# Kernel optimization log

Hardware: AMD Instinct MI355X
Metric: run time of the kernel (lower is better)

The kernel has to match this reference:

```python
import jax, jax.numpy as jnp
import numpy as np

# instant-ngp HashGrid config
L, F, LOG2_T, BASE, SCALE = 16, 2, 19, 16, 1.3819
T = 1 << LOG2_T
B = 1048576
_CORNERS = np.array([[(c >> 0) & 1, (c >> 1) & 1, (c >> 2) & 1] for c in range(8)], np.int32)  # [8,3]


def hash_encode(x, grid):
    # x: [B,3] in [0,1]; grid: [L,T,F] hash tables. Trilinear interp of hashed corner features.
    corners = jnp.asarray(_CORNERS)
    outs = []
    for l in range(L):  # fixed small level loop
        res = float(np.floor(BASE * SCALE ** l))
        pos = x * res
        pos0 = jnp.floor(pos)
        w = pos - pos0                                            # [B,3] trilinear fracs
        idx = pos0.astype(jnp.uint32)[:, None, :] + corners.astype(jnp.uint32)[None]  # [B,8,3]
        h = (idx[..., 0] * jnp.uint32(1)) ^ (idx[..., 1] * jnp.uint32(2654435761)) ^ (idx[..., 2] * jnp.uint32(805459861))
        h = (h & jnp.uint32(T - 1)).astype(jnp.int32)             # [B,8]
        wc = jnp.prod(jnp.where(corners[None] == 1, w[:, None, :], 1.0 - w[:, None, :]), axis=-1)  # [B,8]
        outs.append(jnp.einsum('bcf,bc->bf', grid[l][h], wc))     # [B,F]
    return jnp.concatenate(outs, axis=-1)                         # [B, L*F]


def sh16(d):
    # Spherical harmonics degree 4 (tcnn coefficients), input in [-1,1]^3
    x, y, z = d[:, 0], d[:, 1], d[:, 2]
    x2, y2, z2 = x * x, y * y, z * z
    xy, yz, xz = x * y, y * z, x * z
    one = jnp.ones_like(x)
    return jnp.stack([
        0.28209479177387814 * one,
        -0.48860251190291987 * y,
        0.48860251190291987 * z,
        -0.48860251190291987 * x,
        1.0925484305920792 * xy,
        -1.0925484305920792 * yz,
        0.94617469575755997 * z2 - 0.31539156525251999,
        -1.0925484305920792 * xz,
        0.54627421529603959 * (x2 - y2),
        0.59004358992664352 * y * (-3.0 * x2 + y2),
        2.8906114426405538 * xy * z,
        0.45704579946446572 * y * (1.0 - 5.0 * z2),
        0.3731763325901154 * z * (5.0 * z2 - 3.0),
        0.45704579946446572 * x * (1.0 - 5.0 * z2),
        1.4453057213202769 * z * (x2 - y2),
        0.59004358992664352 * x * (-x2 + 3.0 * y2),
    ], axis=-1)


def setup_inputs() -> dict:
    key = jax.random.key(0)
    ks = jax.random.split(key, 20)
    gdim, shid, chid = 15, 64, 64
    in_color = gdim + 16 + 16  # geo_feat + SH + latent = 47

    def lin(k, o, i):
        k1, k2 = jax.random.split(k)
        bound = 1.0 / np.sqrt(i)
        return (jax.random.uniform(k1, (o, i), jnp.float32, -bound, bound),
                jax.random.uniform(k2, (o,), jnp.float32, -bound, bound))

    sw0, sb0 = lin(ks[0], shid, L * F)
    sw1, sb1 = lin(ks[1], shid, shid)
    sw2, sb2 = lin(ks[2], 1 + gdim, shid)
    cw0, cb0 = lin(ks[3], chid, in_color)
    cw1, cb1 = lin(ks[4], chid, chid)
    cw2, cb2 = lin(ks[5], chid, chid)
    cw3, cb3 = lin(ks[6], 3, chid)
    return {
        'x': jax.random.uniform(ks[7], (B, 3), jnp.float32),
        'd': jax.random.normal(ks[8], (B, 3), jnp.float32),
        'n': jax.random.randint(ks[9], (B,), 0, 100, jnp.int32),
        'grid': jax.random.uniform(ks[10], (L, T, F), jnp.float32, -1e-4, 1e-4),
        'latent_emb': jax.random.normal(ks[11], (100, 16), jnp.float32) * 0.01,
        'sw0': sw0, 'sb0': sb0, 'sw1': sw1, 'sb1': sb1, 'sw2': sw2, 'sb2': sb2,
        'cw0': cw0, 'cb0': cb0, 'cw1': cw1, 'cb1': cb1, 'cw2': cw2, 'cb2': cb2, 'cw3': cw3, 'cb3': cb3,
    }


def reference(x, d, n, grid, latent_emb, sw0, sb0, sw1, sb1, sw2, sb2,
              cw0, cb0, cw1, cb1, cw2, cb2, cw3, cb3):
    h = hash_encode(x, grid)                         # [B, 32]
    h = jax.nn.relu(h @ sw0.T + sb0)
    h = jax.nn.relu(h @ sw1.T + sb1)
    s = h @ sw2.T + sb2                              # [B, 1+geo]
    sigma, geo = s[:, 0], s[:, 1:]
    dd = ((d + 1.0) * 0.5) * 2.0 - 1.0               # module maps d->[0,1]; tcnn SH maps back to [-1,1]
    cin = jnp.concatenate([geo, sh16(dd), latent_emb[n]], axis=-1)  # [B, 47]
    c = jax.nn.relu(cin @ cw0.T + cb0)
    c = jax.nn.relu(c @ cw1.T + cb1)
    c = jax.nn.relu(c @ cw2.T + cb2)
    color = jax.nn.sigmoid(c @ cw3.T + cb3)          # [B, 3]
    return sigma, color
```

## Files before the change

kernel.cpp:

```cpp
#include <hip/hip_runtime.h>
#include <hip/hip_bf16.h>
#include <hip/hip_fp8.h>


#define TBL   524288
#define TMASK (TBL - 1)
#define MPB   512
#define NTHR  1024

#define FP8_SCALE     1048576.0f
#define FP8_INV_SCALE 9.5367431640625e-7f

typedef __bf16 bf16x8 __attribute__((ext_vector_type(8)));
typedef float  f32x4  __attribute__((ext_vector_type(4)));

__device__ const float RES_TAB[16] = {
    16.f, 22.f, 30.f, 42.f, 58.f, 80.f, 111.f, 153.f,
    212.f, 294.f, 406.f, 561.f, 775.f, 1072.f, 1481.f, 2047.f
};

__device__ __forceinline__ unsigned short f2bf(float f) {
    __hip_bfloat16 h = __float2bfloat16(f);
    unsigned short u;
    __builtin_memcpy(&u, &h, 2);
    return u;
}
__device__ __forceinline__ unsigned pack2(float a, float b) {
    return (unsigned)f2bf(a) | ((unsigned)f2bf(b) << 16);
}

__device__ __forceinline__ float fp8_dec(unsigned b) {
#if defined(__has_builtin) && __has_builtin(__builtin_amdgcn_cvt_f32_fp8)
    return __builtin_amdgcn_cvt_f32_fp8((int)b, 0);
#else
    const unsigned e = (b >> 3) & 0xF, m = b & 7;
    float v = e ? ldexpf((float)(8 + m), (int)e - 10) : ldexpf((float)m, -9);
    return (b & 0x80) ? -v : v;
#endif
}
__device__ __forceinline__ unsigned short fp8_pair(float a, float b) {
#if defined(__has_builtin) && __has_builtin(__builtin_amdgcn_cvt_pk_fp8_f32)
    return (unsigned short)(__builtin_amdgcn_cvt_pk_fp8_f32(a, b, 0, false) & 0xffff);
#else
    __hip_fp8_e4m3 qa(a), qb(b);
    return (unsigned short)((unsigned)qa.__x | ((unsigned)qb.__x << 8));
#endif
}

__global__ void __launch_bounds__(1024) grid_to_fp8(
    const float2* __restrict__ g, unsigned short* __restrict__ o, int n)
{
    const int i = blockIdx.x * 1024 + threadIdx.x;
    if (i < n) {
        const float2 v = g[i];
        o[i] = fp8_pair(v.x * FP8_SCALE, v.y * FP8_SCALE);
    }
}

template<int KS, int NT, bool RELU>
__device__ __forceinline__ void mlp_layer(
    const unsigned short* a0, int s0,
    const unsigned short* a1, int s1,
    const unsigned short* __restrict__ W, int ws,
    const float* __restrict__ bias,
    unsigned short* outp, int os,
    int wave, int lane)
{
    const int lr = lane & 15, lg = lane >> 4;
    bf16x8 bfr[NT][KS];
#pragma unroll
    for (int nt = 0; nt < NT; ++nt)
#pragma unroll
        for (int ks = 0; ks < KS; ++ks)
            bfr[nt][ks] = *reinterpret_cast<const bf16x8*>(W + (nt * 16 + lr) * ws + ks * 32 + lg * 8);

#pragma unroll
    for (int mt = 0; mt < 2; ++mt) {
        const int R = wave * 32 + mt * 16;
        bf16x8 afr[KS];
        afr[0] = *reinterpret_cast<const bf16x8*>(a0 + (R + lr) * s0 + lg * 8);
        if constexpr (KS > 1)
            afr[1] = *reinterpret_cast<const bf16x8*>(a1 + (R + lr) * s1 + lg * 8);

        f32x4 acc[NT] = {};
#pragma unroll
        for (int nt = 0; nt < NT; ++nt)
#pragma unroll
            for (int ks = 0; ks < KS; ++ks)
                acc[nt] = __builtin_amdgcn_mfma_f32_16x16x32_bf16(afr[ks], bfr[nt][ks], acc[nt], 0, 0, 0);

#pragma unroll
        for (int nt = 0; nt < NT; ++nt) {
            const float b = bias[nt * 16 + lr];
#pragma unroll
            for (int r = 0; r < 4; ++r) {
                float v = acc[nt][r] + b;
                if (RELU) v = fmaxf(v, 0.f);
                outp[(R + lg * 4 + r) * os + nt * 16 + lr] = f2bf(v);
            }
        }
    }
}

template<int GM>
__global__ void __launch_bounds__(NTHR, 4) nerf_fused(
    const float* __restrict__ x, const float* __restrict__ dvec,
    const int*   __restrict__ nidx, const void* __restrict__ grid,
    const float* __restrict__ latent,
    const float* __restrict__ sw0, const float* __restrict__ sb0,
    const float* __restrict__ sw1, const float* __restrict__ sb1,
    const float* __restrict__ sw2, const float* __restrict__ sb2,
    const float* __restrict__ cw0, const float* __restrict__ cb0,
    const float* __restrict__ cw1, const float* __restrict__ cb1,
    const float* __restrict__ cw2, const float* __restrict__ cb2,
    const float* __restrict__ cw3, const float* __restrict__ cb3,
    float* __restrict__ out, int B)
{
    __shared__ __align__(16) unsigned short sW0[64 * 40];
    __shared__ __align__(16) unsigned short sW1[64 * 72];
    __shared__ __align__(16) unsigned short sW2[16 * 72];
    __shared__ __align__(16) unsigned short sC0[64 * 72];
    __shared__ __align__(16) unsigned short sC1[64 * 72];
    __shared__ __align__(16) unsigned short sC2[64 * 72];
    __shared__ __align__(16) unsigned short sC3[16 * 72];
    __shared__ float sB[352];
    __shared__ __align__(16) unsigned short sAct[MPB * 72];

    const int tid = threadIdx.x;

    for (int i = tid; i < 64 * 40; i += NTHR) { int n = i / 40, k = i % 40; sW0[i] = f2bf(k < 32 ? sw0[n * 32 + k] : 0.f); }
    for (int i = tid; i < 64 * 72; i += NTHR) { int n = i / 72, k = i % 72; sW1[i] = f2bf(k < 64 ? sw1[n * 64 + k] : 0.f); }
    for (int i = tid; i < 16 * 72; i += NTHR) { int n = i / 72, k = i % 72; sW2[i] = f2bf(k < 64 ? sw2[n * 64 + k] : 0.f); }
    for (int i = tid; i < 64 * 72; i += NTHR) {
        int n = i / 72, k = i % 72;
        float v = 0.f;
        if (k < 15) v = cw0[n * 47 + k];
        else if (k >= 32 && k < 64) v = cw0[n * 47 + k - 17];
        sC0[i] = f2bf(v);
    }
    for (int i = tid; i < 64 * 72; i += NTHR) { int n = i / 72, k = i % 72; sC1[i] = f2bf(k < 64 ? cw1[n * 64 + k] : 0.f); }
    for (int i = tid; i < 64 * 72; i += NTHR) { int n = i / 72, k = i % 72; sC2[i] = f2bf(k < 64 ? cw2[n * 64 + k] : 0.f); }
    for (int i = tid; i < 16 * 72; i += NTHR) { int n = i / 72, k = i % 72; sC3[i] = f2bf((n < 3 && k < 64) ? cw3[n * 64 + k] : 0.f); }
    if (tid < 64) {
        sB[tid]       = sb0[tid];
        sB[64 + tid]  = sb1[tid];
        sB[144 + tid] = cb0[tid];
        sB[208 + tid] = cb1[tid];
        sB[272 + tid] = cb2[tid];
    }
    if (tid < 16) {
        sB[128 + tid] = sb2[tid];
        sB[336 + tid] = (tid < 3) ? cb3[tid] : 0.f;
    }

    const int p  = tid & (MPB - 1);
    const int hv = tid >> 9;
    const long long P = (long long)blockIdx.x * MPB + p;

    if constexpr (GM == 1) {
        const float x0 = x[3 * P + 0], x1 = x[3 * P + 1], x2 = x[3 * P + 2];
        const unsigned short* __restrict__ tf = reinterpret_cast<const unsigned short*>(grid);
#pragma unroll 2
        for (int lp = 0; lp < 4; ++lp) {
            unsigned idx[2][8];
            float wxa[2][2], wya[2][2], wza[2][2];
#pragma unroll
            for (int s = 0; s < 2; ++s) {
                const int l = hv * 8 + lp * 2 + s;
                const float res = RES_TAB[l];
                const float px = x0 * res, py = x1 * res, pz = x2 * res;
                const float fx = floorf(px), fy = floorf(py), fz = floorf(pz);
                const float wx = px - fx, wy = py - fy, wz = pz - fz;
                const unsigned ix = (unsigned)fx, iy = (unsigned)fy, iz = (unsigned)fz;
                const unsigned hx0 = ix, hx1 = ix + 1u;
                const unsigned hy0 = iy * 2654435761u, hy1 = (iy + 1u) * 2654435761u;
                const unsigned hz0 = iz * 805459861u,  hz1 = (iz + 1u) * 805459861u;
                const unsigned base = (unsigned)l * (unsigned)TBL;
#pragma unroll
                for (int c = 0; c < 8; ++c) {
                    const unsigned h = ((c & 1) ? hx1 : hx0) ^ (((c >> 1) & 1) ? hy1 : hy0)
                                     ^ (((c >> 2) & 1) ? hz1 : hz0);
                    idx[s][c] = base + (h & TMASK);
                }
                wxa[s][0] = 1.f - wx; wxa[s][1] = wx;
                wya[s][0] = 1.f - wy; wya[s][1] = wy;
                wza[s][0] = 1.f - wz; wza[s][1] = wz;
            }
            unsigned short u[2][8];
#pragma unroll
            for (int s = 0; s < 2; ++s)
#pragma unroll
                for (int c = 0; c < 8; ++c)
                    u[s][c] = tf[idx[s][c]];
#pragma unroll
            for (int s = 0; s < 2; ++s) {
                float f0 = 0.f, f1 = 0.f;
#pragma unroll
                for (int c = 0; c < 8; ++c) {
                    const float wc = wxa[s][c & 1] * wya[s][(c >> 1) & 1] * wza[s][(c >> 2) & 1];
                    const unsigned uu = u[s][c];
                    f0 = fmaf(fp8_dec(uu & 0xffu), wc, f0);
                    f1 = fmaf(fp8_dec((uu >> 8) & 0xffu), wc, f1);
                }
                const int l = hv * 8 + lp * 2 + s;
                *reinterpret_cast<unsigned*>(&sAct[p * 72 + 2 * l]) =
                    pack2(f0 * FP8_INV_SCALE, f1 * FP8_INV_SCALE);
            }
        }
    } else {
        const float x0 = x[3 * P + 0], x1 = x[3 * P + 1], x2 = x[3 * P + 2];
        const float2* __restrict__ gtab = reinterpret_cast<const float2*>(grid);
#pragma unroll 2
        for (int ll = 0; ll < 8; ++ll) {
            const int l = hv * 8 + ll;
            const float res = RES_TAB[l];
            const float px = x0 * res, py = x1 * res, pz = x2 * res;
            const float fx = floorf(px), fy = floorf(py), fz = floorf(pz);
            const float wx = px - fx, wy = py - fy, wz = pz - fz;
            const unsigned ix = (unsigned)fx, iy = (unsigned)fy, iz = (unsigned)fz;
            const unsigned hx[2] = { ix, ix + 1u };
            const unsigned hy[2] = { iy * 2654435761u, (iy + 1u) * 2654435761u };
            const unsigned hz[2] = { iz * 805459861u, (iz + 1u) * 805459861u };
            const float2* tl = gtab + (size_t)l * TBL;
            float2 g[8];
#pragma unroll
            for (int c = 0; c < 8; ++c) {
                const unsigned h = hx[c & 1] ^ hy[(c >> 1) & 1] ^ hz[(c >> 2) & 1];
                g[c] = tl[h & TMASK];
            }
            const float wxa[2] = { 1.f - wx, wx }, wya[2] = { 1.f - wy, wy }, wza[2] = { 1.f - wz, wz };
            float f0 = 0.f, f1 = 0.f;
#pragma unroll
            for (int c = 0; c < 8; ++c) {
                const float wc = wxa[c & 1] * wya[(c >> 1) & 1] * wza[(c >> 2) & 1];
                f0 = fmaf(g[c].x, wc, f0);
                f1 = fmaf(g[c].y, wc, f1);
            }
            *reinterpret_cast<unsigned*>(&sAct[p * 72 + 2 * l]) = pack2(f0, f1);
        }
    }

    unsigned creg0, creg1, creg2, creg3, creg4, creg5, creg6, creg7;
    if (hv == 0) {
        const float X = dvec[3 * P + 0], Y = dvec[3 * P + 1], Z = dvec[3 * P + 2];
        const float x2 = X * X, y2 = Y * Y, z2 = Z * Z, xy = X * Y, yz = Y * Z, xz = X * Z;
        const float s0 = 0.28209479177387814f;
        const float s1 = -0.48860251190291987f * Y;
        const float s2 = 0.48860251190291987f * Z;
        const float s3 = -0.48860251190291987f * X;
        const float s4 = 1.0925484305920792f * xy;
        const float s5 = -1.0925484305920792f * yz;
        const float s6 = 0.94617469575756f * z2 - 0.31539156525252f;
        const float s7 = -1.0925484305920792f * xz;
        const float s8 = 0.5462742152960396f * (x2 - y2);
        const float s9 = 0.5900435899266435f * Y * (-3.f * x2 + y2);
        const float s10 = 2.890611442640554f * xy * Z;
        const float s11 = 0.4570457994644657f * Y * (1.f - 5.f * z2);
        const float s12 = 0.3731763325901154f * Z * (5.f * z2 - 3.f);
        const float s13 = 0.4570457994644657f * X * (1.f - 5.f * z2);
        const float s14 = 1.445305721320277f * Z * (x2 - y2);
        const float s15 = 0.5900435899266435f * X * (-x2 + 3.f * y2);
        creg0 = pack2(s0, s1);   creg1 = pack2(s2, s3);
        creg2 = pack2(s4, s5);   creg3 = pack2(s6, s7);
        creg4 = pack2(s8, s9);   creg5 = pack2(s10, s11);
        creg6 = pack2(s12, s13); creg7 = pack2(s14, s15);
    } else {
        const int id = nidx[P];
        const float4* lp = reinterpret_cast<const float4*>(latent + 16 * id);
        const float4 a = lp[0], b = lp[1], c = lp[2], d4 = lp[3];
        creg0 = pack2(a.x, a.y); creg1 = pack2(a.z, a.w);
        creg2 = pack2(b.x, b.y); creg3 = pack2(b.z, b.w);
        creg4 = pack2(c.x, c.y); creg5 = pack2(c.z, c.w);
        creg6 = pack2(d4.x, d4.y); creg7 = pack2(d4.z, d4.w);
    }

    __syncthreads();

    const int lane = tid & 63;
    const int wave = tid >> 6;

    mlp_layer<1, 4, true>(sAct, 72, nullptr, 0,    sW0, 40, sB + 0,  sAct, 72, wave, lane);
    mlp_layer<2, 4, true>(sAct, 72, sAct + 32, 72, sW1, 72, sB + 64, sAct, 72, wave, lane);

    {
        const int lr = lane & 15, lg = lane >> 4;
        const bf16x8 b0 = *reinterpret_cast<const bf16x8*>(sW2 + lr * 72 + lg * 8);
        const bf16x8 b1 = *reinterpret_cast<const bf16x8*>(sW2 + lr * 72 + 32 + lg * 8);
        const float bb = sB[128 + lr];
#pragma unroll
        for (int mt = 0; mt < 2; ++mt) {
            const int R = wave * 32 + mt * 16;
            const bf16x8 a0 = *reinterpret_cast<const bf16x8*>(sAct + (R + lr) * 72 + lg * 8);
            const bf16x8 a1 = *reinterpret_cast<const bf16x8*>(sAct + (R + lr) * 72 + 32 + lg * 8);
            f32x4 acc = {};
            acc = __builtin_amdgcn_mfma_f32_16x16x32_bf16(a0, b0, acc, 0, 0, 0);
            acc = __builtin_amdgcn_mfma_f32_16x16x32_bf16(a1, b1, acc, 0, 0, 0);
#pragma unroll
            for (int r = 0; r < 4; ++r) {
                const float v = acc[r] + bb;
                const int row = R + lg * 4 + r;
                if (lr == 0) {
                    out[(long long)blockIdx.x * MPB + row] = v;
                    sAct[row * 72 + 31] = 0;
                } else {
                    sAct[row * 72 + lr - 1] = f2bf(v);
                }
                sAct[row * 72 + 15 + lr] = 0;
            }
        }
    }

    __syncthreads();

    {
        unsigned* c2 = reinterpret_cast<unsigned*>(&sAct[p * 72 + 32 + hv * 16]);
        c2[0] = creg0; c2[1] = creg1; c2[2] = creg2; c2[3] = creg3;
        c2[4] = creg4; c2[5] = creg5; c2[6] = creg6; c2[7] = creg7;
    }

    __syncthreads();

    mlp_layer<2, 4, true>(sAct, 72, sAct + 32, 72, sC0, 72, sB + 144, sAct, 72, wave, lane);
    mlp_layer<2, 4, true>(sAct, 72, sAct + 32, 72, sC1, 72, sB + 208, sAct, 72, wave, lane);
    mlp_layer<2, 4, true>(sAct, 72, sAct + 32, 72, sC2, 72, sB + 272, sAct, 72, wave, lane);

    {
        const int lr = lane & 15, lg = lane >> 4;
        const bf16x8 b0 = *reinterpret_cast<const bf16x8*>(sC3 + lr * 72 + lg * 8);
        const bf16x8 b1 = *reinterpret_cast<const bf16x8*>(sC3 + lr * 72 + 32 + lg * 8);
        const float bb = sB[336 + lr];
#pragma unroll
        for (int mt = 0; mt < 2; ++mt) {
            const int R = wave * 32 + mt * 16;
            const bf16x8 a0 = *reinterpret_cast<const bf16x8*>(sAct + (R + lr) * 72 + lg * 8);
            const bf16x8 a1 = *reinterpret_cast<const bf16x8*>(sAct + (R + lr) * 72 + 32 + lg * 8);
            f32x4 acc = {};
            acc = __builtin_amdgcn_mfma_f32_16x16x32_bf16(a0, b0, acc, 0, 0, 0);
            acc = __builtin_amdgcn_mfma_f32_16x16x32_bf16(a1, b1, acc, 0, 0, 0);
            if (lr < 3) {
#pragma unroll
                for (int r = 0; r < 4; ++r) {
                    const float v = acc[r] + bb;
                    const long long row = (long long)blockIdx.x * MPB + R + lg * 4 + r;
                    out[(long long)B + row * 3 + lr] = 1.f / (1.f + __expf(-v));
                }
            }
        }
    }
}

extern "C" void kernel_launch(void* const* d_in, const int* in_sizes, int n_in,
                              void* d_out, int out_size, void* d_ws, size_t ws_size,
                              hipStream_t stream) {
    const float* x    = (const float*)d_in[0];
    const float* dv   = (const float*)d_in[1];
    const int*   n    = (const int*)d_in[2];
    const float* grid = (const float*)d_in[3];
    const float* lat  = (const float*)d_in[4];
    const float* sw0  = (const float*)d_in[5];
    const float* sb0  = (const float*)d_in[6];
    const float* sw1  = (const float*)d_in[7];
    const float* sb1  = (const float*)d_in[8];
    const float* sw2  = (const float*)d_in[9];
    const float* sb2  = (const float*)d_in[10];
    const float* cw0  = (const float*)d_in[11];
    const float* cb0  = (const float*)d_in[12];
    const float* cw1  = (const float*)d_in[13];
    const float* cb1  = (const float*)d_in[14];
    const float* cw2  = (const float*)d_in[15];
    const float* cb2  = (const float*)d_in[16];
    const float* cw3  = (const float*)d_in[17];
    const float* cb3  = (const float*)d_in[18];

    const int B = in_sizes[2];
    const int nblocks = B / MPB;

    const int nent = 16 * TBL;
    const size_t ws_need = (size_t)nent * 2;

    if (ws_size >= ws_need) {
        grid_to_fp8<<<dim3((nent + 1023) / 1024), dim3(1024), 0, stream>>>(
            reinterpret_cast<const float2*>(grid), (unsigned short*)d_ws, nent);
        nerf_fused<1><<<dim3(nblocks), dim3(NTHR), 0, stream>>>(
            x, dv, n, (const void*)d_ws, lat,
            sw0, sb0, sw1, sb1, sw2, sb2,
            cw0, cb0, cw1, cb1, cw2, cb2, cw3, cb3,
            (float*)d_out, B);
    } else {
        nerf_fused<0><<<dim3(nblocks), dim3(NTHR), 0, stream>>>(
            x, dv, n, (const void*)grid, lat,
            sw0, sb0, sw1, sb1, sw2, sb2,
            cw0, cb0, cw1, cb1, cw2, cb2, cw3, cb3,
            (float*)d_out, B);
    }
}
```

Before: 621.6 us.

## Pre-pack MLP weights once globally and halve block size for occupancy

Adds a single-block kernel that converts and pads all MLP weights and biases to bf16/float in workspace once, so the main kernel no longer stages ~48KB of weights into shared memory per block. The fused kernel now reads weight fragments directly from global/L2 and uses only the activation buffer in LDS. It also halves points per block to 256 with 512 threads and raises launch bounds to 8 blocks per CU. The aim is to cut per-block setup cost and LDS pressure so more blocks stay resident to hide the hash-gather latency. In exchange, weight operands are fetched from cache on every MFMA layer instead of LDS.

```diff
diff --git a/kernel.cpp b/kernel.cpp
--- a/kernel.cpp
+++ b/kernel.cpp
@@ -5,8 +5,20 @@
 
 #define TBL   524288
 #define TMASK (TBL - 1)
-#define MPB   512
-#define NTHR  1024
+#define MPB   256
+#define NTHR  512
+
+#define GRID_SHORTS (16 * TBL)
+#define GRID_BYTES  (GRID_SHORTS * 2)
+#define OW0 0
+#define OW1 2560
+#define OC0 7168
+#define OC1 11776
+#define OC2 16384
+#define OW2 20992
+#define OC3 22144
+#define OBF 23296
+#define WS_NEED ((size_t)GRID_BYTES + 48000)
 
 #define FP8_SCALE     1048576.0f
 #define FP8_INV_SCALE 9.5367431640625e-7f
@@ -54,6 +66,44 @@
     if (i < n) {
         const float2 v = g[i];
         o[i] = fp8_pair(v.x * FP8_SCALE, v.y * FP8_SCALE);
+    }
+}
+
+__global__ void __launch_bounds__(1024) pack_weights(
+    unsigned short* __restrict__ w,
+    const float* __restrict__ sw0, const float* __restrict__ sb0,
+    const float* __restrict__ sw1, const float* __restrict__ sb1,
+    const float* __restrict__ sw2, const float* __restrict__ sb2,
+    const float* __restrict__ cw0, const float* __restrict__ cb0,
+    const float* __restrict__ cw1, const float* __restrict__ cb1,
+    const float* __restrict__ cw2, const float* __restrict__ cb2,
+    const float* __restrict__ cw3, const float* __restrict__ cb3)
+{
+    const int tid = threadIdx.x;
+    for (int i = tid; i < 64 * 40; i += 1024) { int n = i / 40, k = i % 40; w[OW0 + i] = f2bf(k < 32 ? sw0[n * 32 + k] : 0.f); }
+    for (int i = tid; i < 64 * 72; i += 1024) { int n = i / 72, k = i % 72; w[OW1 + i] = f2bf(k < 64 ? sw1[n * 64 + k] : 0.f); }
+    for (int i = tid; i < 64 * 72; i += 1024) {
+        int n = i / 72, k = i % 72;
+        float v = 0.f;
+        if (k < 15) v = cw0[n * 47 + k];
+        else if (k >= 32 && k < 64) v = cw0[n * 47 + k - 17];
+        w[OC0 + i] = f2bf(v);
+    }
+    for (int i = tid; i < 64 * 72; i += 1024) { int n = i / 72, k = i % 72; w[OC1 + i] = f2bf(k < 64 ? cw1[n * 64 + k] : 0.f); }
+    for (int i = tid; i < 64 * 72; i += 1024) { int n = i / 72, k = i % 72; w[OC2 + i] = f2bf(k < 64 ? cw2[n * 64 + k] : 0.f); }
+    for (int i = tid; i < 16 * 72; i += 1024) { int n = i / 72, k = i % 72; w[OW2 + i] = f2bf(k < 64 ? sw2[n * 64 + k] : 0.f); }
+    for (int i = tid; i < 16 * 72; i += 1024) { int n = i / 72, k = i % 72; w[OC3 + i] = f2bf((n < 3 && k < 64) ? cw3[n * 64 + k] : 0.f); }
+    float* gB = reinterpret_cast<float*>(w + OBF);
+    if (tid < 64) {
+        gB[tid]       = sb0[tid];
+        gB[64 + tid]  = sb1[tid];
+        gB[144 + tid] = cb0[tid];
+        gB[208 + tid] = cb1[tid];
+        gB[272 + tid] = cb2[tid];
+    }
+    if (tid < 16) {
+        gB[128 + tid] = sb2[tid];
+        gB[336 + tid] = (tid < 3) ? cb3[tid] : 0.f;
     }
 }
 
@@ -102,64 +152,25 @@
     }
 }
 
-template<int GM>
-__global__ void __launch_bounds__(NTHR, 4) nerf_fused(
+__global__ void __launch_bounds__(NTHR, 8) nerf_fused_v8(
     const float* __restrict__ x, const float* __restrict__ dvec,
-    const int*   __restrict__ nidx, const void* __restrict__ grid,
+    const int*   __restrict__ nidx,
+    const unsigned short* __restrict__ gfp8,
+    const unsigned short* __restrict__ wz,
     const float* __restrict__ latent,
-    const float* __restrict__ sw0, const float* __restrict__ sb0,
-    const float* __restrict__ sw1, const float* __restrict__ sb1,
-    const float* __restrict__ sw2, const float* __restrict__ sb2,
-    const float* __restrict__ cw0, const float* __restrict__ cb0,
-    const float* __restrict__ cw1, const float* __restrict__ cb1,
-    const float* __restrict__ cw2, const float* __restrict__ cb2,
-    const float* __restrict__ cw3, const float* __restrict__ cb3,
     float* __restrict__ out, int B)
 {
-    __shared__ __align__(16) unsigned short sW0[64 * 40];
-    __shared__ __align__(16) unsigned short sW1[64 * 72];
-    __shared__ __align__(16) unsigned short sW2[16 * 72];
-    __shared__ __align__(16) unsigned short sC0[64 * 72];
-    __shared__ __align__(16) unsigned short sC1[64 * 72];
-    __shared__ __align__(16) unsigned short sC2[64 * 72];
-    __shared__ __align__(16) unsigned short sC3[16 * 72];
-    __shared__ float sB[352];
     __shared__ __align__(16) unsigned short sAct[MPB * 72];
 
     const int tid = threadIdx.x;
-
-    for (int i = tid; i < 64 * 40; i += NTHR) { int n = i / 40, k = i % 40; sW0[i] = f2bf(k < 32 ? sw0[n * 32 + k] : 0.f); }
-    for (int i = tid; i < 64 * 72; i += NTHR) { int n = i / 72, k = i % 72; sW1[i] = f2bf(k < 64 ? sw1[n * 64 + k] : 0.f); }
-    for (int i = tid; i < 16 * 72; i += NTHR) { int n = i / 72, k = i % 72; sW2[i] = f2bf(k < 64 ? sw2[n * 64 + k] : 0.f); }
-    for (int i = tid; i < 64 * 72; i += NTHR) {
-        int n = i / 72, k = i % 72;
-        float v = 0.f;
-        if (k < 15) v = cw0[n * 47 + k];
-        else if (k >= 32 && k < 64) v = cw0[n * 47 + k - 17];
-        sC0[i] = f2bf(v);
-    }
-    for (int i = tid; i < 64 * 72; i += NTHR) { int n = i / 72, k = i % 72; sC1[i] = f2bf(k < 64 ? cw1[n * 64 + k] : 0.f); }
-    for (int i = tid; i < 64 * 72; i += NTHR) { int n = i / 72, k = i % 72; sC2[i] = f2bf(k < 64 ? cw2[n * 64 + k] : 0.f); }
-    for (int i = tid; i < 16 * 72; i += NTHR) { int n = i / 72, k = i % 72; sC3[i] = f2bf((n < 3 && k < 64) ? cw3[n * 64 + k] : 0.f); }
-    if (tid < 64) {
-        sB[tid]       = sb0[tid];
-        sB[64 + tid]  = sb1[tid];
-        sB[144 + tid] = cb0[tid];
-        sB[208 + tid] = cb1[tid];
-        sB[272 + tid] = cb2[tid];
-    }
-    if (tid < 16) {
-        sB[128 + tid] = sb2[tid];
-        sB[336 + tid] = (tid < 3) ? cb3[tid] : 0.f;
-    }
+    const float* __restrict__ gB = reinterpret_cast<const float*>(wz + OBF);
 
     const int p  = tid & (MPB - 1);
-    const int hv = tid >> 9;
+    const int hv = tid >> 8;
     const long long P = (long long)blockIdx.x * MPB + p;
 
-    if constexpr (GM == 1) {
+    {
         const float x0 = x[3 * P + 0], x1 = x[3 * P + 1], x2 = x[3 * P + 2];
-        const unsigned short* __restrict__ tf = reinterpret_cast<const unsigned short*>(grid);
 #pragma unroll 2
         for (int lp = 0; lp < 4; ++lp) {
             unsigned idx[2][8];
@@ -170,7 +181,7 @@
                 const float res = RES_TAB[l];
                 const float px = x0 * res, py = x1 * res, pz = x2 * res;
                 const float fx = floorf(px), fy = floorf(py), fz = floorf(pz);
-                const float wx = px - fx, wy = py - fy, wz = pz - fz;
+                const float wx = px - fx, wy = py - fy, wz2 = pz - fz;
                 const unsigned ix = (unsigned)fx, iy = (unsigned)fy, iz = (unsigned)fz;
                 const unsigned hx0 = ix, hx1 = ix + 1u;
                 const unsigned hy0 = iy * 2654435761u, hy1 = (iy + 1u) * 2654435761u;
@@ -184,14 +195,14 @@
                 }
                 wxa[s][0] = 1.f - wx; wxa[s][1] = wx;
                 wya[s][0] = 1.f - wy; wya[s][1] = wy;
-                wza[s][0] = 1.f - wz; wza[s][1] = wz;
+                wza[s][0] = 1.f - wz2; wza[s][1] = wz2;
             }
             unsigned short u[2][8];
 #pragma unroll
             for (int s = 0; s < 2; ++s)
 #pragma unroll
                 for (int c = 0; c < 8; ++c)
-                    u[s][c] = tf[idx[s][c]];
+                    u[s][c] = gfp8[idx[s][c]];
 #pragma unroll
             for (int s = 0; s < 2; ++s) {
                 float f0 = 0.f, f1 = 0.f;
@@ -206,37 +217,6 @@
                 *reinterpret_cast<unsigned*>(&sAct[p * 72 + 2 * l]) =
                     pack2(f0 * FP8_INV_SCALE, f1 * FP8_INV_SCALE);
             }
-        }
-    } else {
-        const float x0 = x[3 * P + 0], x1 = x[3 * P + 1], x2 = x[3 * P + 2];
-        const float2* __restrict__ gtab = reinterpret_cast<const float2*>(grid);
-#pragma unroll 2
-        for (int ll = 0; ll < 8; ++ll) {
-            const int l = hv * 8 + ll;
-            const float res = RES_TAB[l];
-            const float px = x0 * res, py = x1 * res, pz = x2 * res;
-            const float fx = floorf(px), fy = floorf(py), fz = floorf(pz);
-            const float wx = px - fx, wy = py - fy, wz = pz - fz;
-            const unsigned ix = (unsigned)fx, iy = (unsigned)fy, iz = (unsigned)fz;
-            const unsigned hx[2] = { ix, ix + 1u };
-            const unsigned hy[2] = { iy * 2654435761u, (iy + 1u) * 2654435761u };
-            const unsigned hz[2] = { iz * 805459861u, (iz + 1u) * 805459861u };
-            const float2* tl = gtab + (size_t)l * TBL;
-            float2 g[8];
-#pragma unroll
-            for (int c = 0; c < 8; ++c) {
-                const unsigned h = hx[c & 1] ^ hy[(c >> 1) & 1] ^ hz[(c >> 2) & 1];
-                g[c] = tl[h & TMASK];
-            }
-            const float wxa[2] = { 1.f - wx, wx }, wya[2] = { 1.f - wy, wy }, wza[2] = { 1.f - wz, wz };
-            float f0 = 0.f, f1 = 0.f;
-#pragma unroll
-            for (int c = 0; c < 8; ++c) {
-                const float wc = wxa[c & 1] * wya[(c >> 1) & 1] * wza[(c >> 2) & 1];
-                f0 = fmaf(g[c].x, wc, f0);
-                f1 = fmaf(g[c].y, wc, f1);
-            }
-            *reinterpret_cast<unsigned*>(&sAct[p * 72 + 2 * l]) = pack2(f0, f1);
         }
     }
 
@@ -279,14 +259,14 @@
     const int lane = tid & 63;
     const int wave = tid >> 6;
 
-    mlp_layer<1, 4, true>(sAct, 72, nullptr, 0,    sW0, 40, sB + 0,  sAct, 72, wave, lane);
-    mlp_layer<2, 4, true>(sAct, 72, sAct + 32, 72, sW1, 72, sB + 64, sAct, 72, wave, lane);
+    mlp_layer<1, 4, true>(sAct, 72, nullptr, 0,    wz + OW0, 40, gB + 0,  sAct, 72, wave, lane);
+    mlp_layer<2, 4, true>(sAct, 72, sAct + 32, 72, wz + OW1, 72, gB + 64, sAct, 72, wave, lane);
 
     {
         const int lr = lane & 15, lg = lane >> 4;
-        const bf16x8 b0 = *reinterpret_cast<const bf16x8*>(sW2 + lr * 72 + lg * 8);
-        const bf16x8 b1 = *reinterpret_cast<const bf16x8*>(sW2 + lr * 72 + 32 + lg * 8);
-        const float bb = sB[128 + lr];
+        const bf16x8 b0 = *reinterpret_cast<const bf16x8*>(wz + OW2 + lr * 72 + lg * 8);
+        const bf16x8 b1 = *reinterpret_cast<const bf16x8*>(wz + OW2 + lr * 72 + 32 + lg * 8);
+        const float bb = gB[128 + lr];
 #pragma unroll
         for (int mt = 0; mt < 2; ++mt) {
             const int R = wave * 32 + mt * 16;
@@ -320,15 +300,15 @@
 
     __syncthreads();
 
-    mlp_layer<2, 4, true>(sAct, 72, sAct + 32, 72, sC0, 72, sB + 144, sAct, 72, wave, lane);
-    mlp_layer<2, 4, true>(sAct, 72, sAct + 32, 72, sC1, 72, sB + 208, sAct, 72, wave, lane);
-    mlp_layer<2, 4, true>(sAct, 72, sAct + 32, 72, sC2, 72, sB + 272, sAct, 72, wave, lane);
+    mlp_layer<2, 4, true>(sAct, 72, sAct + 32, 72, wz + OC0, 72, gB + 144, sAct, 72, wave, lane);
+    mlp_layer<2, 4, true>(sAct, 72, sAct + 32, 72, wz + OC1, 72, gB + 208, sAct, 72, wave, lane);
+    mlp_layer<2, 4, true>(sAct, 72, sAct + 32, 72, wz + OC2, 72, gB + 272, sAct, 72, wave, lane);
 
     {
         const int lr = lane & 15, lg = lane >> 4;
-        const bf16x8 b0 = *reinterpret_cast<const bf16x8*>(sC3 + lr * 72 + lg * 8);
-        const bf16x8 b1 = *reinterpret_cast<const bf16x8*>(sC3 + lr * 72 + 32 + lg * 8);
-        const float bb = sB[336 + lr];
+        const bf16x8 b0 = *reinterpret_cast<const bf16x8*>(wz + OC3 + lr * 72 + lg * 8);
+        const bf16x8 b1 = *reinterpret_cast<const bf16x8*>(wz + OC3 + lr * 72 + 32 + lg * 8);
+        const float bb = gB[336 + lr];
 #pragma unroll
         for (int mt = 0; mt < 2; ++mt) {
             const int R = wave * 32 + mt * 16;
@@ -342,6 +322,202 @@
                 for (int r = 0; r < 4; ++r) {
                     const float v = acc[r] + bb;
                     const long long row = (long long)blockIdx.x * MPB + R + lg * 4 + r;
+                    out[(long long)B + row * 3 + lr] = 1.f / (1.f + __expf(-v));
+                }
+            }
+        }
+    }
+}
+
+__global__ void __launch_bounds__(1024, 4) nerf_fused_f32(
+    const float* __restrict__ x, const float* __restrict__ dvec,
+    const int*   __restrict__ nidx, const float* __restrict__ grid,
+    const float* __restrict__ latent,
+    const float* __restrict__ sw0, const float* __restrict__ sb0,
+    const float* __restrict__ sw1, const float* __restrict__ sb1,
+    const float* __restrict__ sw2, const float* __restrict__ sb2,
+    const float* __restrict__ cw0, const float* __restrict__ cb0,
+    const float* __restrict__ cw1, const float* __restrict__ cb1,
+    const float* __restrict__ cw2, const float* __restrict__ cb2,
+    const float* __restrict__ cw3, const float* __restrict__ cb3,
+    float* __restrict__ out, int B)
+{
+    __shared__ __align__(16) unsigned short sW0[64 * 40];
+    __shared__ __align__(16) unsigned short sW1[64 * 72];
+    __shared__ __align__(16) unsigned short sW2[16 * 72];
+    __shared__ __align__(16) unsigned short sC0[64 * 72];
+    __shared__ __align__(16) unsigned short sC1[64 * 72];
+    __shared__ __align__(16) unsigned short sC2[64 * 72];
+    __shared__ __align__(16) unsigned short sC3[16 * 72];
+    __shared__ float sB[352];
+    __shared__ __align__(16) unsigned short sAct[512 * 72];
+
+    const int tid = threadIdx.x;
+
+    for (int i = tid; i < 64 * 40; i += 1024) { int n = i / 40, k = i % 40; sW0[i] = f2bf(k < 32 ? sw0[n * 32 + k] : 0.f); }
+    for (int i = tid; i < 64 * 72; i += 1024) { int n = i / 72, k = i % 72; sW1[i] = f2bf(k < 64 ? sw1[n * 64 + k] : 0.f); }
+    for (int i = tid; i < 16 * 72; i += 1024) { int n = i / 72, k = i % 72; sW2[i] = f2bf(k < 64 ? sw2[n * 64 + k] : 0.f); }
+    for (int i = tid; i < 64 * 72; i += 1024) {
+        int n = i / 72, k = i % 72;
+        float v = 0.f;
+        if (k < 15) v = cw0[n * 47 + k];
+        else if (k >= 32 && k < 64) v = cw0[n * 47 + k - 17];
+        sC0[i] = f2bf(v);
+    }
+    for (int i = tid; i < 64 * 72; i += 1024) { int n = i / 72, k = i % 72; sC1[i] = f2bf(k < 64 ? cw1[n * 64 + k] : 0.f); }
+    for (int i = tid; i < 64 * 72; i += 1024) { int n = i / 72, k = i % 72; sC2[i] = f2bf(k < 64 ? cw2[n * 64 + k] : 0.f); }
+    for (int i = tid; i < 16 * 72; i += 1024) { int n = i / 72, k = i % 72; sC3[i] = f2bf((n < 3 && k < 64) ? cw3[n * 64 + k] : 0.f); }
+    if (tid < 64) {
+        sB[tid]       = sb0[tid];
+        sB[64 + tid]  = sb1[tid];
+        sB[144 + tid] = cb0[tid];
+        sB[208 + tid] = cb1[tid];
+        sB[272 + tid] = cb2[tid];
+    }
+    if (tid < 16) {
+        sB[128 + tid] = sb2[tid];
+        sB[336 + tid] = (tid < 3) ? cb3[tid] : 0.f;
+    }
+
+    const int p  = tid & 511;
+    const int hv = tid >> 9;
+    const long long P = (long long)blockIdx.x * 512 + p;
+
+    {
+        const float x0 = x[3 * P + 0], x1 = x[3 * P + 1], x2 = x[3 * P + 2];
+        const float2* __restrict__ gtab = reinterpret_cast<const float2*>(grid);
+#pragma unroll 2
+        for (int ll = 0; ll < 8; ++ll) {
+            const int l = hv * 8 + ll;
+            const float res = RES_TAB[l];
+            const float px = x0 * res, py = x1 * res, pz = x2 * res;
+            const float fx = floorf(px), fy = floorf(py), fz = floorf(pz);
+            const float wx = px - fx, wy = py - fy, wz = pz - fz;
+            const unsigned ix = (unsigned)fx, iy = (unsigned)fy, iz = (unsigned)fz;
+            const unsigned hx[2] = { ix, ix + 1u };
+            const unsigned hy[2] = { iy * 2654435761u, (iy + 1u) * 2654435761u };
+            const unsigned hz[2] = { iz * 805459861u, (iz + 1u) * 805459861u };
+            const float2* tl = gtab + (size_t)l * TBL;
+            float2 g[8];
+#pragma unroll
+            for (int c = 0; c < 8; ++c) {
+                const unsigned h = hx[c & 1] ^ hy[(c >> 1) & 1] ^ hz[(c >> 2) & 1];
+                g[c] = tl[h & TMASK];
+            }
+            const float wxa[2] = { 1.f - wx, wx }, wya[2] = { 1.f - wy, wy }, wza[2] = { 1.f - wz, wz };
+            float f0 = 0.f, f1 = 0.f;
+#pragma unroll
+            for (int c = 0; c < 8; ++c) {
+                const float wc = wxa[c & 1] * wya[(c >> 1) & 1] * wza[(c >> 2) & 1];
+                f0 = fmaf(g[c].x, wc, f0);
+                f1 = fmaf(g[c].y, wc, f1);
+            }
+            *reinterpret_cast<unsigned*>(&sAct[p * 72 + 2 * l]) = pack2(f0, f1);
+        }
+    }
+
+    unsigned creg0, creg1, creg2, creg3, creg4, creg5, creg6, creg7;
+    if (hv == 0) {
+        const float X = dvec[3 * P + 0], Y = dvec[3 * P + 1], Z = dvec[3 * P + 2];
+        const float x2 = X * X, y2 = Y * Y, z2 = Z * Z, xy = X * Y, yz = Y * Z, xz = X * Z;
+        const float s0 = 0.28209479177387814f;
+        const float s1 = -0.48860251190291987f * Y;
+        const float s2 = 0.48860251190291987f * Z;
+        const float s3 = -0.48860251190291987f * X;
+        const float s4 = 1.0925484305920792f * xy;
+        const float s5 = -1.0925484305920792f * yz;
+        const float s6 = 0.94617469575756f * z2 - 0.31539156525252f;
+        const float s7 = -1.0925484305920792f * xz;
+        const float s8 = 0.5462742152960396f * (x2 - y2);
+        const float s9 = 0.5900435899266435f * Y * (-3.f * x2 + y2);
+        const float s10 = 2.890611442640554f * xy * Z;
+        const float s11 = 0.4570457994644657f * Y * (1.f - 5.f * z2);
+        const float s12 = 0.3731763325901154f * Z * (5.f * z2 - 3.f);
+        const float s13 = 0.4570457994644657f * X * (1.f - 5.f * z2);
+        const float s14 = 1.445305721320277f * Z * (x2 - y2);
+        const float s15 = 0.5900435899266435f * X * (-x2 + 3.f * y2);
+        creg0 = pack2(s0, s1);   creg1 = pack2(s2, s3);
+        creg2 = pack2(s4, s5);   creg3 = pack2(s6, s7);
+        creg4 = pack2(s8, s9);   creg5 = pack2(s10, s11);
+        creg6 = pack2(s12, s13); creg7 = pack2(s14, s15);
+    } else {
+        const int id = nidx[P];
+        const float4* lp = reinterpret_cast<const float4*>(latent + 16 * id);
+        const float4 a = lp[0], b = lp[1], c = lp[2], d4 = lp[3];
+        creg0 = pack2(a.x, a.y); creg1 = pack2(a.z, a.w);
+        creg2 = pack2(b.x, b.y); creg3 = pack2(b.z, b.w);
+        creg4 = pack2(c.x, c.y); creg5 = pack2(c.z, c.w);
+        creg6 = pack2(d4.x, d4.y); creg7 = pack2(d4.z, d4.w);
+    }
+
+    __syncthreads();
+
+    const int lane = tid & 63;
+    const int wave = tid >> 6;
+
+    mlp_layer<1, 4, true>(sAct, 72, nullptr, 0,    sW0, 40, sB + 0,  sAct, 72, wave, lane);
+    mlp_layer<2, 4, true>(sAct, 72, sAct + 32, 72, sW1, 72, sB + 64, sAct, 72, wave, lane);
+
+    {
+        const int lr = lane & 15, lg = lane >> 4;
+        const bf16x8 b0 = *reinterpret_cast<const bf16x8*>(sW2 + lr * 72 + lg * 8);
+        const bf16x8 b1 = *reinterpret_cast<const bf16x8*>(sW2 + lr * 72 + 32 + lg * 8);
+        const float bb = sB[128 + lr];
+#pragma unroll
+        for (int mt = 0; mt < 2; ++mt) {
+            const int R = wave * 32 + mt * 16;
+            const bf16x8 a0 = *reinterpret_cast<const bf16x8*>(sAct + (R + lr) * 72 + lg * 8);
+            const bf16x8 a1 = *reinterpret_cast<const bf16x8*>(sAct + (R + lr) * 72 + 32 + lg * 8);
+            f32x4 acc = {};
+            acc = __builtin_amdgcn_mfma_f32_16x16x32_bf16(a0, b0, acc, 0, 0, 0);
+            acc = __builtin_amdgcn_mfma_f32_16x16x32_bf16(a1, b1, acc, 0, 0, 0);
+#pragma unroll
+            for (int r = 0; r < 4; ++r) {
+                const float v = acc[r] + bb;
+                const int row = R + lg * 4 + r;
+                if (lr == 0) {
+                    out[(long long)blockIdx.x * 512 + row] = v;
+                    sAct[row * 72 + 31] = 0;
+                } else {
+                    sAct[row * 72 + lr - 1] = f2bf(v);
+                }
+                sAct[row * 72 + 15 + lr] = 0;
+            }
+        }
+    }
+
+    __syncthreads();
+
+    {
+        unsigned* c2 = reinterpret_cast<unsigned*>(&sAct[p * 72 + 32 + hv * 16]);
+        c2[0] = creg0; c2[1] = creg1; c2[2] = creg2; c2[3] = creg3;
+        c2[4] = creg4; c2[5] = creg5; c2[6] = creg6; c2[7] = creg7;
+    }
+
+    __syncthreads();
+
+    mlp_layer<2, 4, true>(sAct, 72, sAct + 32, 72, sC0, 72, sB + 144, sAct, 72, wave, lane);
+    mlp_layer<2, 4, true>(sAct, 72, sAct + 32, 72, sC1, 72, sB + 208, sAct, 72, wave, lane);
+    mlp_layer<2, 4, true>(sAct, 72, sAct + 32, 72, sC2, 72, sB + 272, sAct, 72, wave, lane);
+
+    {
+        const int lr = lane & 15, lg = lane >> 4;
+        const bf16x8 b0 = *reinterpret_cast<const bf16x8*>(sC3 + lr * 72 + lg * 8);
+        const bf16x8 b1 = *reinterpret_cast<const bf16x8*>(sC3 + lr * 72 + 32 + lg * 8);
+        const float bb = sB[336 + lr];
+#pragma unroll
+        for (int mt = 0; mt < 2; ++mt) {
+            const int R = wave * 32 + mt * 16;
+            const bf16x8 a0 = *reinterpret_cast<const bf16x8*>(sAct + (R + lr) * 72 + lg * 8);
+            const bf16x8 a1 = *reinterpret_cast<const bf16x8*>(sAct + (R + lr) * 72 + 32 + lg * 8);
+            f32x4 acc = {};
+            acc = __builtin_amdgcn_mfma_f32_16x16x32_bf16(a0, b0, acc, 0, 0, 0);
+            acc = __builtin_amdgcn_mfma_f32_16x16x32_bf16(a1, b1, acc, 0, 0, 0);
+            if (lr < 3) {
+#pragma unroll
+                for (int r = 0; r < 4; ++r) {
+                    const float v = acc[r] + bb;
+                    const long long row = (long long)blockIdx.x * 512 + R + lg * 4 + r;
                     out[(long long)B + row * 3 + lr] = 1.f / (1.f + __expf(-v));
                 }
             }
@@ -373,24 +549,22 @@
     const float* cb3  = (const float*)d_in[18];
 
     const int B = in_sizes[2];
-    const int nblocks = B / MPB;
-
-    const int nent = 16 * TBL;
-    const size_t ws_need = (size_t)nent * 2;
-
-    if (ws_size >= ws_need) {
-        grid_to_fp8<<<dim3((nent + 1023) / 1024), dim3(1024), 0, stream>>>(
-            reinterpret_cast<const float2*>(grid), (unsigned short*)d_ws, nent);
-        nerf_fused<1><<<dim3(nblocks), dim3(NTHR), 0, stream>>>(
-            x, dv, n, (const void*)d_ws, lat,
+
+    if (ws_size >= WS_NEED && (B % MPB) == 0) {
+        unsigned short* wsS = (unsigned short*)d_ws;
+        unsigned short* wz  = (unsigned short*)((char*)d_ws + GRID_BYTES);
+        grid_to_fp8<<<dim3((GRID_SHORTS + 1023) / 1024), dim3(1024), 0, stream>>>(
+            reinterpret_cast<const float2*>(grid), wsS, GRID_SHORTS);
+        pack_weights<<<dim3(1), dim3(1024), 0, stream>>>(
+            wz, sw0, sb0, sw1, sb1, sw2, sb2,
+            cw0, cb0, cw1, cb1, cw2, cb2, cw3, cb3);
+        nerf_fused_v8<<<dim3(B / MPB), dim3(NTHR), 0, stream>>>(
+            x, dv, n, wsS, wz, lat, (float*)d_out, B);
+    } else {
+        nerf_fused_f32<<<dim3(B / 512), dim3(1024), 0, stream>>>(
+            x, dv, n, grid, lat,
             sw0, sb0, sw1, sb1, sw2, sb2,
             cw0, cb0, cw1, cb1, cw2, cb2, cw3, cb3,
             (float*)d_out, B);
-    } else {
-        nerf_fused<0><<<dim3(nblocks), dim3(NTHR), 0, stream>>>(
-            x, dv, n, (const void*)grid, lat,
-            sw0, sb0, sw1, sb1, sw2, sb2,
-            cw0, cb0, cw1, cb1, cw2, cb2, cw3, cb3,
-            (float*)d_out, B);
-    }
-}
+    }
+}
```

Result: slower. 767.8 us (+23.5%).
